# Optimization experiments

Hardware: AMD Instinct MI355X
Metric: run time of the kernel (lower is better)

Reference implementation:

```python
import jax, jax.numpy as jnp
import numpy as np

EMBED_DIM = 768
NUM_HEADS = 12
HEAD_DIM = EMBED_DIM // NUM_HEADS
KERNEL = 7


def _neighbor_index(size, kernel):
    # NATTEN border-clamped neighborhood: window start = clip(i - k//2, 0, size-k)
    start = np.clip(np.arange(size) - kernel // 2, 0, size - kernel)
    return jnp.asarray(start[:, None] + np.arange(kernel)[None, :])  # [size, kernel]


def setup_inputs() -> dict:
    key = jax.random.key(0)
    k1, k2, k3, k4, k5 = jax.random.split(key, 5)
    B, H, W, C = 8, 64, 64, EMBED_DIM
    x = jax.random.normal(k1, (B, H, W, C), dtype=jnp.float32)
    # torch.nn.Linear layout: weight [out, in]
    w_qkv = jax.random.normal(k2, (3 * C, C), dtype=jnp.float32) * (C ** -0.5)
    b_qkv = jax.random.normal(k3, (3 * C,), dtype=jnp.float32) * 0.02
    w_proj = jax.random.normal(k4, (C, C), dtype=jnp.float32) * (C ** -0.5)
    b_proj = jax.random.normal(k5, (C,), dtype=jnp.float32) * 0.02
    return {"x": x, "w_qkv": w_qkv, "b_qkv": b_qkv, "w_proj": w_proj, "b_proj": b_proj}


def reference(x, w_qkv, b_qkv, w_proj, b_proj):
    B, H, W, C = x.shape
    scale = HEAD_DIM ** -0.5
    qkv = (x @ w_qkv.T + b_qkv).reshape(B, H, W, 3, NUM_HEADS, HEAD_DIM)
    q = qkv[..., 0, :, :] * scale          # [B,H,W,nh,hd]
    k = qkv[..., 1, :, :]
    v = qkv[..., 2, :, :]

    idx_i = _neighbor_index(H, KERNEL)      # [H,K]
    idx_j = _neighbor_index(W, KERNEL)      # [W,K]

    # Logits over the K*K local neighborhood, one shifted gather per offset
    # (avoids materializing [B,H,W,K2,nh,hd]).
    logits = []
    for ki in range(KERNEL):
        k_row = jnp.take(k, idx_i[:, ki], axis=1)          # [B,H,W,nh,hd]
        for kj in range(KERNEL):
            k_nb = jnp.take(k_row, idx_j[:, kj], axis=2)   # [B,H,W,nh,hd]
            logits.append(jnp.einsum('bhwnd,bhwnd->bhwn', q, k_nb))
    logits = jnp.stack(logits, axis=-1)                     # [B,H,W,nh,K2]
    attn = jax.nn.softmax(logits, axis=-1)

    out = jnp.zeros((B, H, W, NUM_HEADS, HEAD_DIM), dtype=x.dtype)
    off = 0
    for ki in range(KERNEL):
        v_row = jnp.take(v, idx_i[:, ki], axis=1)
        for kj in range(KERNEL):
            v_nb = jnp.take(v_row, idx_j[:, kj], axis=2)
            out = out + attn[..., off][..., None] * v_nb
            off += 1

    out = out.reshape(B, H, W, C)
    return out @ w_proj.T + b_proj
```

## Files before the change

### kernel.cpp

```cpp
#include <hip/hip_runtime.h>
#include <cstddef>

#define EMBED   768
#define NHEADS  12
#define HDIM    64
#define KSZ     7
#define IMG_H   64
#define IMG_W   64
#define BATCH   8
#define NTOK    (BATCH*IMG_H*IMG_W)
#define QKV_N   (3*EMBED)

typedef __attribute__((ext_vector_type(8))) short  bf16x8;
typedef __attribute__((ext_vector_type(4))) float  f32x4;
typedef __attribute__((ext_vector_type(8))) unsigned short u16x8;
typedef __attribute__((ext_vector_type(4))) unsigned short u16x4;

__device__ __forceinline__ unsigned short f2bf(float f) {
    unsigned int u = __float_as_uint(f);
    u += 0x7FFFu + ((u >> 16) & 1u);
    return (unsigned short)(u >> 16);
}

__device__ __forceinline__ void gload_lds16(const void* g, void* l) {
    __builtin_amdgcn_global_load_lds(
        (const __attribute__((address_space(1))) unsigned int*)g,
        (__attribute__((address_space(3))) unsigned int*)l, 16, 0, 0);
}

__global__ __launch_bounds__(256)
void cvt_all_kernel(const float* __restrict__ x, const float* __restrict__ wq,
                    const float* __restrict__ wp, unsigned short* __restrict__ xbf,
                    unsigned short* __restrict__ wqbf, unsigned short* __restrict__ wpbf)
{
    const int NX = NTOK * EMBED / 4;
    const int NQ = QKV_N * EMBED / 4;
    const int NP = EMBED * EMBED / 4;
    int i = blockIdx.x * 256 + threadIdx.x;
    const float* src; unsigned short* dst; int j;
    if (i < NX)           { src = x;  dst = xbf;  j = i; }
    else if (i < NX + NQ) { src = wq; dst = wqbf; j = i - NX; }
    else if (i < NX + NQ + NP) { src = wp; dst = wpbf; j = i - NX - NQ; }
    else return;
    float4 f = *(const float4*)(src + (size_t)j * 4);
    u16x4 o;
    o[0] = f2bf(f.x); o[1] = f2bf(f.y); o[2] = f2bf(f.z); o[3] = f2bf(f.w);
    *(u16x4*)(dst + (size_t)j * 4) = o;
}

template<int BF16OUT>
__global__ __launch_bounds__(512)
void gemm256(const unsigned short* __restrict__ A, const unsigned short* __restrict__ W,
             const float* __restrict__ bias, void* __restrict__ outp,
             int M, int N, int K, int scaleN, float scale)
{
    __shared__ unsigned short lds[65536];
    const int t_ = threadIdx.x;
    const int l = t_ & 63, w = t_ >> 6;
    const int wm = w >> 2, wn = w & 3;

    const int nby = N >> 8;
    const int xcd = blockIdx.x & 7;
    const int loc = blockIdx.x >> 3;
    const int bmg = loc / nby;
    int bnq = loc - bmg * nby;
    if (bmg & 1) bnq = nby - 1 - bnq;
    const int bm = (xcd * (((M >> 8) >> 3)) + bmg) << 8;
    const int bn = bnq << 8;

    const int kperm8 = ((l & 3) ^ ((l >> 3) & 3)) * 8;
    const unsigned short* gA = A + (size_t)(bm + w * 16 + (l >> 2)) * K + kperm8;
    const unsigned short* gB = W + (size_t)(bn + w * 16 + (l >> 2)) * K + kperm8;
    const size_t rstep = (size_t)128 * K;

    const int foff = (l & 15) * 32 + (((l >> 4) ^ ((l >> 1) & 3)) * 8);
    const int aoff = wm * 8 * 512;
    const int boff = 8192 + wn * 4 * 512;

    f32x4 acc[8][4] = {};
    const int NT = K / 32;

#define BARRIER() asm volatile("s_barrier" ::: "memory")
#define WAITV8()  asm volatile("s_waitcnt vmcnt(8)" ::: "memory")
#define WAITV4()  asm volatile("s_waitcnt vmcnt(4)" ::: "memory")
#define WAITV0()  asm volatile("s_waitcnt vmcnt(0)" ::: "memory")
#define STG(tt) do { \
        const int cc_ = ((tt) & 3) * 16384; const size_t ko_ = (size_t)(tt) * 32; \
        gload_lds16(gA + ko_,         lds + cc_ + w * 512); \
        gload_lds16(gA + rstep + ko_, lds + cc_ + (w + 8) * 512); \
        gload_lds16(gB + ko_,         lds + cc_ + 8192 + w * 512); \
        gload_lds16(gB + rstep + ko_, lds + cc_ + 8192 + (w + 8) * 512); } while (0)

    STG(0); STG(1); STG(2);
    WAITV8();
    BARRIER();

    for (int t = 0; t < NT; ++t) {
        const int c = (t & 3) * 16384;
        bf16x8 a[4], bq[4];

        #pragma unroll
        for (int m = 0; m < 4; ++m) a[m]  = *(const bf16x8*)(lds + c + aoff + m * 512 + foff);
        #pragma unroll
        for (int n = 0; n < 4; ++n) bq[n] = *(const bf16x8*)(lds + c + boff + n * 512 + foff);
        BARRIER();
        __builtin_amdgcn_s_setprio(1);
        #pragma unroll
        for (int m = 0; m < 4; ++m)
            #pragma unroll
            for (int n = 0; n < 4; ++n)
                acc[m][n] = __builtin_amdgcn_mfma_f32_16x16x32_bf16(a[m], bq[n], acc[m][n], 0, 0, 0);
        __builtin_amdgcn_s_setprio(0);

        #pragma unroll
        for (int m = 0; m < 4; ++m) a[m] = *(const bf16x8*)(lds + c + aoff + (4 + m) * 512 + foff);
        if (t + 3 < NT)      { STG(t + 3); WAITV8(); }
        else if (t == NT - 3)  WAITV4();
        else if (t == NT - 2)  WAITV0();
        BARRIER();
        __builtin_amdgcn_s_setprio(1);
        #pragma unroll
        for (int m = 0; m < 4; ++m)
            #pragma unroll
            for (int n = 0; n < 4; ++n)
                acc[4 + m][n] = __builtin_amdgcn_mfma_f32_16x16x32_bf16(a[m], bq[n], acc[4 + m][n], 0, 0, 0);
        __builtin_amdgcn_s_setprio(0);
    }
#undef BARRIER
#undef WAITV8
#undef WAITV4
#undef WAITV0
#undef STG

    const int cr = (l >> 4) * 4;
    const int cc = l & 15;
    #pragma unroll
    for (int m = 0; m < 8; ++m) {
        #pragma unroll
        for (int n = 0; n < 4; ++n) {
            const int col = bn + wn * 64 + n * 16 + cc;
            const float bv = bias[col];
            const bool sc = col < scaleN;
            #pragma unroll
            for (int r = 0; r < 4; ++r) {
                const int row = bm + wm * 128 + m * 16 + cr + r;
                float v = acc[m][n][r] + bv;
                if (sc) v *= scale;
                if (BF16OUT) ((unsigned short*)outp)[(size_t)row * N + col] = f2bf(v);
                else         ((float*)outp)[(size_t)row * N + col] = v;
            }
        }
    }
}

__global__ __launch_bounds__(256)
void natten_kernel(const unsigned short* __restrict__ qkv, unsigned short* __restrict__ attn_bf)
{
    __shared__ unsigned short smem[4 * 5888];
    const int t = threadIdx.x;
    const int w = t >> 6, l = t & 63;
    const int c15 = l & 15, g = l >> 4;
    const int blk = blockIdx.x;
    const int tg = blk & 15;
    const int h = (blk >> 4) % NHEADS;
    const int b = blk / (16 * NHEADS);
    const int ti = (tg >> 2) * 16, tj = (tg & 3) * 16;
    const int pi0 = ti + w * 4;
    const int ws = min(max(pi0 - 3, 0), IMG_H - 10);
    const int cs = min(max(tj - 3, 0), IMG_W - 22);
    const int pixbase = b * 4096;

    unsigned short* Kl = smem + w * 5888;
    unsigned short* Vt = Kl + 2304;

    const int pj = tj + c15;
    const int sj = min(max(pj - 3, 0), IMG_W - KSZ);
    const unsigned int cm = 0x7Fu << (sj - cs);
    unsigned int rm[4];
    #pragma unroll
    for (int qt = 0; qt < 4; ++qt) {
        int si = min(max(pi0 + qt - 3, 0), IMG_H - KSZ);
        rm[qt] = 0x7Fu << (si - ws);
    }

    bf16x8 qf[4][2];
    #pragma unroll
    for (int qt = 0; qt < 4; ++qt)
        #pragma unroll
        for (int dh = 0; dh < 2; ++dh)
            qf[qt][dh] = *(const bf16x8*)(qkv +
                (size_t)(pixbase + (pi0 + qt) * 64 + tj + c15) * QKV_N + h * HDIM + dh * 32 + g * 8);

    const int sr = l & 31;
    const int h5 = l >> 5;
    const int sig = ((sr & 12) << 1) | ((sr & 16) >> 2) | (sr & 3);

    u16x8 kst[4], vst[4];

    {
        int ur = sr / 22, uc = sr - ur * 22;
        int prow = min(ws + ur, IMG_H - 1);
        const u16x8* gk = (const u16x8*)(qkv +
            (size_t)(pixbase + prow * 64 + cs + uc) * QKV_N + EMBED + h * HDIM + h5 * 32);
        #pragma unroll
        for (int i = 0; i < 4; ++i) { kst[i] = gk[i]; vst[i] = gk[i + 96]; }
    }
    #pragma unroll
    for (int i = 0; i < 4; ++i) *(u16x8*)(Kl + sr * 72 + h5 * 32 + i * 8) = kst[i];
    #pragma unroll
    for (int i = 0; i < 4; ++i)
        #pragma unroll
        for (int e = 0; e < 8; ++e)
            Vt[(h5 * 32 + i * 8 + e) * 56 + sig] = vst[i][e];

    f32x4 oacc[4][4] = {};
    float spart[4] = {0.f, 0.f, 0.f, 0.f};

    #pragma unroll 1
    for (int C = 0; C < 7; ++C) {
        if (C < 6) {
            int kk = (C + 1) * 32 + sr;
            int ur = kk / 22, uc = kk - ur * 22;
            int prow = min(ws + ur, IMG_H - 1);
            const u16x8* gk = (const u16x8*)(qkv +
                (size_t)(pixbase + prow * 64 + cs + uc) * QKV_N + EMBED + h * HDIM + h5 * 32);
            #pragma unroll
            for (int i = 0; i < 4; ++i) { kst[i] = gk[i]; vst[i] = gk[i + 96]; }
        }

        bf16x8 ka[2][2], vb[4];
        #pragma unroll
        for (int kt = 0; kt < 2; ++kt)
            #pragma unroll
            for (int dh = 0; dh < 2; ++dh)
                ka[kt][dh] = *(const bf16x8*)(Kl + (kt * 16 + c15) * 72 + dh * 32 + g * 8);
        #pragma unroll
        for (int dt = 0; dt < 4; ++dt)
            vb[dt] = *(const bf16x8*)(Vt + (dt * 16 + c15) * 56 + g * 8);

        int kk0 = C * 32 + 4 * g;
        int a22 = kk0 / 22;
        int uc0 = kk0 - a22 * 22;
        int urx[2][4]; unsigned int cb[2][4];
        #pragma unroll
        for (int kt = 0; kt < 2; ++kt)
            #pragma unroll
            for (int r = 0; r < 4; ++r) {
                int x = uc0 + kt * 16 + r;
                int wrp = x >= 22;
                int uc = x - (wrp ? 22 : 0);
                urx[kt][r] = a22 + wrp;
                cb[kt][r] = (cm >> uc) & 1u;
            }

        #pragma unroll
        for (int qt = 0; qt < 4; ++qt) {
            f32x4 s0 = {}, s1 = {};
            s0 = __builtin_amdgcn_mfma_f32_16x16x32_bf16(ka[0][0], qf[qt][0], s0, 0, 0, 0);
            s0 = __builtin_amdgcn_mfma_f32_16x16x32_bf16(ka[0][1], qf[qt][1], s0, 0, 0, 0);
            s1 = __builtin_amdgcn_mfma_f32_16x16x32_bf16(ka[1][0], qf[qt][0], s1, 0, 0, 0);
            s1 = __builtin_amdgcn_mfma_f32_16x16x32_bf16(ka[1][1], qf[qt][1], s1, 0, 0, 0);
            float p[2][4];
            #pragma unroll
            for (int r = 0; r < 4; ++r) {
                float e0 = exp2f(s0[r]);
                float e1 = exp2f(s1[r]);
                p[0][r] = ((rm[qt] >> urx[0][r]) & cb[0][r]) ? e0 : 0.f;
                p[1][r] = ((rm[qt] >> urx[1][r]) & cb[1][r]) ? e1 : 0.f;
                spart[qt] += p[0][r] + p[1][r];
            }
            unsigned int pk[4];
            asm("v_cvt_pk_bf16_f32 %0, %1, %2" : "=v"(pk[0]) : "v"(p[0][0]), "v"(p[0][1]));
            asm("v_cvt_pk_bf16_f32 %0, %1, %2" : "=v"(pk[1]) : "v"(p[0][2]), "v"(p[0][3]));
            asm("v_cvt_pk_bf16_f32 %0, %1, %2" : "=v"(pk[2]) : "v"(p[1][0]), "v"(p[1][1]));
            asm("v_cvt_pk_bf16_f32 %0, %1, %2" : "=v"(pk[3]) : "v"(p[1][2]), "v"(p[1][3]));
            bf16x8 pa = *(bf16x8*)pk;
            #pragma unroll
            for (int dt = 0; dt < 4; ++dt)
                oacc[qt][dt] = __builtin_amdgcn_mfma_f32_16x16x32_bf16(pa, vb[dt], oacc[qt][dt], 0, 0, 0);
        }

        if (C < 6) {
            #pragma unroll
            for (int i = 0; i < 4; ++i) *(u16x8*)(Kl + sr * 72 + h5 * 32 + i * 8) = kst[i];
            #pragma unroll
            for (int i = 0; i < 4; ++i)
                #pragma unroll
                for (int e = 0; e < 8; ++e)
                    Vt[(h5 * 32 + i * 8 + e) * 56 + sig] = vst[i][e];
        }
    }

    #pragma unroll
    for (int qt = 0; qt < 4; ++qt) {
        float s = spart[qt];
        s += __shfl_xor(s, 16);
        s += __shfl_xor(s, 32);
        #pragma unroll
        for (int r = 0; r < 4; ++r) {
            float sb = __shfl(s, 4 * g + r);
            float inv = __builtin_amdgcn_rcpf(sb);
            size_t obase = (size_t)(pixbase + (pi0 + qt) * 64 + tj + 4 * g + r) * EMBED
                         + h * HDIM + c15;
            #pragma unroll
            for (int dt = 0; dt < 4; ++dt)
                attn_bf[obase + dt * 16] = f2bf(oacc[qt][dt][r] * inv);
        }
    }
}

extern "C" void kernel_launch(void* const* d_in, const int* in_sizes, int n_in,
                              void* d_out, int out_size, void* d_ws, size_t ws_size,
                              hipStream_t stream)
{
    const float* x      = (const float*)d_in[0];
    const float* w_qkv  = (const float*)d_in[1];
    const float* b_qkv  = (const float*)d_in[2];
    const float* w_proj = (const float*)d_in[3];
    const float* b_proj = (const float*)d_in[4];
    float* out = (float*)d_out;

    char* p = (char*)d_ws;
    unsigned short* qkv = (unsigned short*)p;     p += (size_t)NTOK * QKV_N * 2;
    unsigned short* xbf = (unsigned short*)p;
    unsigned short* attn_bf = xbf;                p += (size_t)NTOK * EMBED * 2;
    unsigned short* wq_bf = (unsigned short*)p;   p += (size_t)QKV_N * EMBED * 2;
    unsigned short* wp_bf = (unsigned short*)p;

    const float scale = 0.125f * 1.44269504088896f;

    {
        const int ntot = (NTOK * EMBED + QKV_N * EMBED + EMBED * EMBED) / 4;
        cvt_all_kernel<<<(ntot + 255) / 256, 256, 0, stream>>>(
            x, w_qkv, w_proj, xbf, wq_bf, wp_bf);
    }

    {
        gemm256<1><<<(NTOK / 256) * (QKV_N / 256), 512, 0, stream>>>(
            xbf, wq_bf, b_qkv, qkv, NTOK, QKV_N, EMBED, EMBED, scale);
    }

    natten_kernel<<<BATCH * NHEADS * 16, 256, 0, stream>>>(qkv, attn_bf);

    {
        gemm256<0><<<(NTOK / 256) * (EMBED / 256), 512, 0, stream>>>(
            attn_bf, wp_bf, b_proj, out, NTOK, EMBED, EMBED, 0, 1.0f);
    }
}
```

Before: 315.3 us.

## Shrink GEMM tile to 256x128 with K=64 double-buffered LDS pipeline

Both projection GEMMs change from a 256x256 output tile with four 32-wide K stages to a 256x128 tile with two 64-wide K buffers. The 8 waves now form a 4x2 grid, and each wave holds 4x4 accumulators instead of 8x4. The aim is to lower register and LDS pressure and to double the number of blocks, which improves occupancy and load balance, especially for the narrow output projection with N=768. In exchange each tile reuses loaded data less and more global traffic is needed for the A operand.

```diff
diff --git a/kernel.cpp b/kernel.cpp
--- a/kernel.cpp
+++ b/kernel.cpp
@@ -50,59 +50,63 @@
 
 template<int BF16OUT>
 __global__ __launch_bounds__(512)
-void gemm256(const unsigned short* __restrict__ A, const unsigned short* __restrict__ W,
-             const float* __restrict__ bias, void* __restrict__ outp,
-             int M, int N, int K, int scaleN, float scale)
+void gemmT(const unsigned short* __restrict__ A, const unsigned short* __restrict__ W,
+           const float* __restrict__ bias, void* __restrict__ outp,
+           int M, int N, int K, int scaleN, float scale)
 {
-    __shared__ unsigned short lds[65536];
+    __shared__ unsigned short lds[49152];
     const int t_ = threadIdx.x;
     const int l = t_ & 63, w = t_ >> 6;
-    const int wm = w >> 2, wn = w & 3;
-
-    const int nby = N >> 8;
+    const int wm = w >> 1, wn = w & 1;
+
+    const int nby = N >> 7;
     const int xcd = blockIdx.x & 7;
     const int loc = blockIdx.x >> 3;
     const int bmg = loc / nby;
     int bnq = loc - bmg * nby;
     if (bmg & 1) bnq = nby - 1 - bnq;
-    const int bm = (xcd * (((M >> 8) >> 3)) + bmg) << 8;
-    const int bn = bnq << 8;
+    const int bm = (xcd * ((M >> 8) >> 3) + bmg) << 8;
+    const int bn = bnq << 7;
 
     const int kperm8 = ((l & 3) ^ ((l >> 3) & 3)) * 8;
-    const unsigned short* gA = A + (size_t)(bm + w * 16 + (l >> 2)) * K + kperm8;
-    const unsigned short* gB = W + (size_t)(bn + w * 16 + (l >> 2)) * K + kperm8;
-    const size_t rstep = (size_t)128 * K;
+    const unsigned short* gA = A + (size_t)(bm + 32 * w + (l >> 2)) * K + kperm8;
+    const unsigned short* gB = W + (size_t)(bn + 16 * w + (l >> 2)) * K + kperm8;
+    const size_t rstepA = (size_t)16 * K;
 
     const int foff = (l & 15) * 32 + (((l >> 4) ^ ((l >> 1) & 3)) * 8);
-    const int aoff = wm * 8 * 512;
-    const int boff = 8192 + wn * 4 * 512;
-
-    f32x4 acc[8][4] = {};
-    const int NT = K / 32;
+    const int aoff = wm * 4096;
+    const int boff = 16384 + wn * 4096;
+
+    f32x4 acc[4][4] = {};
+    const int NT = K / 64;
 
 #define BARRIER() asm volatile("s_barrier" ::: "memory")
-#define WAITV8()  asm volatile("s_waitcnt vmcnt(8)" ::: "memory")
-#define WAITV4()  asm volatile("s_waitcnt vmcnt(4)" ::: "memory")
+#define WAITV3()  asm volatile("s_waitcnt vmcnt(3)" ::: "memory")
 #define WAITV0()  asm volatile("s_waitcnt vmcnt(0)" ::: "memory")
-#define STG(tt) do { \
-        const int cc_ = ((tt) & 3) * 16384; const size_t ko_ = (size_t)(tt) * 32; \
-        gload_lds16(gA + ko_,         lds + cc_ + w * 512); \
-        gload_lds16(gA + rstep + ko_, lds + cc_ + (w + 8) * 512); \
-        gload_lds16(gB + ko_,         lds + cc_ + 8192 + w * 512); \
-        gload_lds16(gB + rstep + ko_, lds + cc_ + 8192 + (w + 8) * 512); } while (0)
-
-    STG(0); STG(1); STG(2);
-    WAITV8();
+#define STGA(c, k0, kk) do { \
+        gload_lds16(gA + (size_t)(k0) + (kk) * 32,          lds + (c) + (4 * w + (kk)) * 512); \
+        gload_lds16(gA + rstepA + (size_t)(k0) + (kk) * 32, lds + (c) + (4 * w + 2 + (kk)) * 512); } while (0)
+#define STGB(c, k0, kk) \
+        gload_lds16(gB + (size_t)(k0) + (kk) * 32, lds + (c) + 16384 + (2 * w + (kk)) * 512)
+
+    STGA(0, 0, 0); STGB(0, 0, 0); STGA(0, 0, 1); STGB(0, 0, 1);
+    WAITV3();
     BARRIER();
 
     for (int t = 0; t < NT; ++t) {
-        const int c = (t & 3) * 16384;
+        const int c  = (t & 1) * 24576;
+        const int cn = c ^ 24576;
+        const int k1 = (t + 1) * 64;
+        const bool pf = (t + 1) < NT;
+
         bf16x8 a[4], bq[4];
 
         #pragma unroll
-        for (int m = 0; m < 4; ++m) a[m]  = *(const bf16x8*)(lds + c + aoff + m * 512 + foff);
-        #pragma unroll
-        for (int n = 0; n < 4; ++n) bq[n] = *(const bf16x8*)(lds + c + boff + n * 512 + foff);
+        for (int m = 0; m < 4; ++m) a[m]  = *(const bf16x8*)(lds + c + aoff + (m * 2) * 512 + foff);
+        #pragma unroll
+        for (int n = 0; n < 4; ++n) bq[n] = *(const bf16x8*)(lds + c + boff + (n * 2) * 512 + foff);
+        if (pf) { STGA(cn, k1, 0); STGB(cn, k1, 0); WAITV3(); }
+        else    { WAITV0(); }
         BARRIER();
         __builtin_amdgcn_s_setprio(1);
         #pragma unroll
@@ -113,29 +117,29 @@
         __builtin_amdgcn_s_setprio(0);
 
         #pragma unroll
-        for (int m = 0; m < 4; ++m) a[m] = *(const bf16x8*)(lds + c + aoff + (4 + m) * 512 + foff);
-        if (t + 3 < NT)      { STG(t + 3); WAITV8(); }
-        else if (t == NT - 3)  WAITV4();
-        else if (t == NT - 2)  WAITV0();
+        for (int m = 0; m < 4; ++m) a[m]  = *(const bf16x8*)(lds + c + aoff + (m * 2 + 1) * 512 + foff);
+        #pragma unroll
+        for (int n = 0; n < 4; ++n) bq[n] = *(const bf16x8*)(lds + c + boff + (n * 2 + 1) * 512 + foff);
+        if (pf) { STGA(cn, k1, 1); STGB(cn, k1, 1); WAITV3(); }
         BARRIER();
         __builtin_amdgcn_s_setprio(1);
         #pragma unroll
         for (int m = 0; m < 4; ++m)
             #pragma unroll
             for (int n = 0; n < 4; ++n)
-                acc[4 + m][n] = __builtin_amdgcn_mfma_f32_16x16x32_bf16(a[m], bq[n], acc[4 + m][n], 0, 0, 0);
+                acc[m][n] = __builtin_amdgcn_mfma_f32_16x16x32_bf16(a[m], bq[n], acc[m][n], 0, 0, 0);
         __builtin_amdgcn_s_setprio(0);
     }
 #undef BARRIER
-#undef WAITV8
-#undef WAITV4
+#undef WAITV3
 #undef WAITV0
-#undef STG
+#undef STGA
+#undef STGB
 
     const int cr = (l >> 4) * 4;
     const int cc = l & 15;
     #pragma unroll
-    for (int m = 0; m < 8; ++m) {
+    for (int m = 0; m < 4; ++m) {
         #pragma unroll
         for (int n = 0; n < 4; ++n) {
             const int col = bn + wn * 64 + n * 16 + cc;
@@ -143,7 +147,7 @@
             const bool sc = col < scaleN;
             #pragma unroll
             for (int r = 0; r < 4; ++r) {
-                const int row = bm + wm * 128 + m * 16 + cr + r;
+                const int row = bm + wm * 64 + m * 16 + cr + r;
                 float v = acc[m][n][r] + bv;
                 if (sc) v *= scale;
                 if (BF16OUT) ((unsigned short*)outp)[(size_t)row * N + col] = f2bf(v);
@@ -336,14 +340,14 @@
     }
 
     {
-        gemm256<1><<<(NTOK / 256) * (QKV_N / 256), 512, 0, stream>>>(
+        gemmT<1><<<(NTOK / 256) * (QKV_N / 128), 512, 0, stream>>>(
             xbf, wq_bf, b_qkv, qkv, NTOK, QKV_N, EMBED, EMBED, scale);
     }
 
     natten_kernel<<<BATCH * NHEADS * 16, 256, 0, stream>>>(qkv, attn_bf);
 
     {
-        gemm256<0><<<(NTOK / 256) * (EMBED / 256), 512, 0, stream>>>(
+        gemmT<0><<<(NTOK / 256) * (EMBED / 128), 512, 0, stream>>>(
             attn_bf, wp_bf, b_proj, out, NTOK, EMBED, EMBED, 0, 1.0f);
     }
 }
```

Result: slower. 331.6 us (+5.2%).
